# Performance work log

Hardware: AMD Instinct MI355X
Metric: run time of the kernel (lower is better)

## Reference

```python
import jax, jax.numpy as jnp
import numpy as np

N_NODES = 100000
N_EDGES = 3200000
D_FEAT = 256
TOP_K = 50000


def setup_inputs() -> dict:
    key = jax.random.key(0)
    k1, k2, k3 = jax.random.split(key, 3)
    h = jax.random.normal(k1, (N_NODES, D_FEAT), dtype=jnp.float32)
    W = jax.random.normal(k2, (D_FEAT, 1), dtype=jnp.float32) * (1.0 / np.sqrt(D_FEAT))
    b = jnp.zeros((1,), dtype=jnp.float32)
    edge_index = jax.random.randint(k3, (2, N_EDGES), 0, N_NODES, dtype=jnp.int64)
    return {"h": h, "W": W, "b": b, "edge_index": edge_index, "top_k": TOP_K}


def reference(h, W, b, edge_index, top_k):
    # scores = sigmoid(Linear(h)) -> [N, 1]
    scores = jax.nn.sigmoid(h @ W + b)  # [N, 1]
    # top-k node selection by score (descending), like dgl.topk_nodes
    top_scores, node_ids = jax.lax.top_k(scores[:, 0], top_k)  # [k], [k]
    # gather features of selected nodes, scale by their scores
    new_h = h[node_ids] * top_scores[:, None]  # [k, d]
    # induced-subgraph edges: edge kept iff both endpoints selected
    member = jnp.zeros((h.shape[0],), dtype=bool).at[node_ids].set(True)
    edge_mask = member[edge_index[0]] & member[edge_index[1]]  # [E]
    return new_h, node_ids, edge_mask
```

## Files before the change

### kernel.cpp

```cpp
#include <hip/hip_runtime.h>
#include <math.h>

#define N_NODES 100000
#define D_FEAT  256
#define TOP_K   50000
#define NBINS   65536
#define NCHUNK  64
#define CUTPOS  (N_NODES - TOP_K)
#define ROWSTRIDE 260


__device__ __forceinline__ int bucket_of(float s) {
    int b = (int)(s * 65536.0f);
    return min(max(b, 0), NBINS - 1);
}

__device__ __forceinline__ float np_expf(float x) {
    float q  = rintf(x * 1.44269504088896341f);
    float xr = fmaf(-q, 0.693359375f, x);
    xr       = fmaf(-q, -2.12194440e-4f, xr);
    float x2 = xr * xr;
    float p  = 1.9875691500E-4f;
    p = fmaf(p, xr, 1.3981999507E-3f);
    p = fmaf(p, xr, 8.3334519073E-3f);
    p = fmaf(p, xr, 4.1665795894E-2f);
    p = fmaf(p, xr, 1.6666665459E-1f);
    p = fmaf(p, xr, 5.0000001201E-1f);
    p = fmaf(p, x2, xr);
    p = p + 1.0f;
    return ldexpf(p, (int)q);
}

__global__ void score_kernel(const float* __restrict__ h,
                             const float* __restrict__ W,
                             const float* __restrict__ bvec,
                             float* __restrict__ s32,
                             int* __restrict__ hist) {
    __shared__ float rows[32 * ROWSTRIDE];
    __shared__ float wl[256];
    int tid  = threadIdx.x;
    int wave = tid >> 6;
    int lane = tid & 63;
    int g    = lane >> 3;
    int l    = lane & 7;

    wl[tid] = W[tid];

    int nodeBase = blockIdx.x * 32 + wave * 8;
#pragma unroll
    for (int r = 0; r < 8; ++r) {
        float4 v = ((const float4*)(h + (size_t)(nodeBase + r) * D_FEAT))[lane];
        *((float4*)&rows[(wave * 8 + r) * ROWSTRIDE + lane * 4]) = v;
    }
    __syncthreads();

    float wreg[32];
#pragma unroll
    for (int i = 0; i < 32; ++i) wreg[i] = wl[i * 8 + l];

    const float* myrow = &rows[(wave * 8 + g) * ROWSTRIDE];
    float acc = 0.0f;
#pragma unroll
    for (int i = 0; i < 32; ++i)
        acc = fmaf(myrow[i * 8 + l], wreg[i], acc);

    float b01 = acc + __shfl_xor(acc, 1, 64);
    float b23 = b01 + __shfl_xor(b01, 2, 64);
    float z   = b23 + __shfl_xor(b23, 4, 64);

    z = z + bvec[0];
    float x = -z;
    float t = np_expf(x);
    float u = 1.0f + t;
    float s = 1.0f / u;

    if (l == 0) {
        int node = nodeBase + g;
        s32[node] = s;
        atomicAdd(&hist[bucket_of(s)], 1);
    }
}

__global__ void scan_chunks_kernel(const int* __restrict__ hist,
                                   int* __restrict__ offs,
                                   int* __restrict__ cursor,
                                   int* __restrict__ chunkSum) {
    __shared__ int wsum[4];
    int tid  = threadIdx.x;
    int lane = tid & 63;
    int wid  = tid >> 6;
    int base = blockIdx.x * 1024 + tid * 4;

    int4 hv = *((const int4*)(hist + base));
    int e1 = hv.x;
    int e2 = hv.x + hv.y;
    int e3 = e2 + hv.z;
    int tot = e3 + hv.w;

    int incl = tot;
#pragma unroll
    for (int d = 1; d < 64; d <<= 1) {
        int t = __shfl_up(incl, d, 64);
        if (lane >= d) incl += t;
    }
    if (lane == 63) wsum[wid] = incl;
    __syncthreads();
    int wbase = 0;
#pragma unroll
    for (int w = 0; w < 3; ++w)
        if (w < wid) wbase += wsum[w];

    int excl = wbase + (incl - tot);
    int4 ov = make_int4(excl, excl + e1, excl + e2, excl + e3);
    *((int4*)(offs + base))   = ov;
    *((int4*)(cursor + base)) = ov;
    if (tid == 255) chunkSum[blockIdx.x] = excl + tot;
}

__device__ __forceinline__ void build_base(const int* __restrict__ chunkSum,
                                           int* sbase, int tid) {
    if (tid < 64) {
        int v = chunkSum[tid];
        int inc = v;
#pragma unroll
        for (int d = 1; d < 64; d <<= 1) {
            int t = __shfl_up(inc, d, 64);
            if (tid >= d) inc += t;
        }
        sbase[tid] = inc - v;
    }
}

__global__ void scatter_kernel(const float* __restrict__ s32,
                               int* __restrict__ cursor,
                               const int* __restrict__ chunkSum,
                               float* __restrict__ ss,
                               int* __restrict__ si) {
    __shared__ int sbase[64];
    int tid = threadIdx.x;
    build_base(chunkSum, sbase, tid);
    __syncthreads();
    int i = blockIdx.x * 256 + tid;
    if (i >= N_NODES) return;
    float s = s32[i];
    int b = bucket_of(s);
    int pos = sbase[b >> 10] + atomicAdd(&cursor[b], 1);
    ss[pos] = s;
    si[pos] = i;
}

__global__ void bucket_sort_kernel(const int* __restrict__ offs,
                                   const int* __restrict__ chunkSum,
                                   float* __restrict__ ss,
                                   int* __restrict__ si) {
    __shared__ int sbase[65];
    int tid = threadIdx.x;
    build_base(chunkSum, sbase, tid);
    if (tid == 64) sbase[64] = N_NODES;
    __syncthreads();
    int b = blockIdx.x * 256 + tid;
    int s0 = sbase[b >> 10] + offs[b];
    int e  = (b == NBINS - 1) ? N_NODES : sbase[(b + 1) >> 10] + offs[b + 1];
    if (e <= CUTPOS || e - s0 < 2) return;
    for (int i = s0 + 1; i < e; ++i) {
        float ks = ss[i];
        int   ki = si[i];
        int j = i - 1;
        while (j >= s0) {
            float ps = ss[j];
            int   pi = si[j];
            bool gt = (ps > ks) || (ps == ks && pi < ki);
            if (!gt) break;
            ss[j + 1] = ps;
            si[j + 1] = pi;
            --j;
        }
        ss[j + 1] = ks;
        si[j + 1] = ki;
    }
}

__global__ void emit_gather_kernel(const float* __restrict__ h,
                                   const float* __restrict__ ss,
                                   const int* __restrict__ si,
                                   float* __restrict__ out_newh,
                                   float* __restrict__ out_ids,
                                   unsigned char* __restrict__ member) {
    int tid  = threadIdx.x;
    int row  = blockIdx.x * 4 + (tid >> 6);
    int lane = tid & 63;
    int p = N_NODES - 1 - row;
    int id  = si[p];
    float s = ss[p];
    if (lane == 0) {
        member[id]   = 1;
        out_ids[row] = (float)id;
    }
    const float4* hv = (const float4*)(h + (size_t)id * D_FEAT);
    float4 v = hv[lane];
    ((float4*)(out_newh + (size_t)row * D_FEAT))[lane] =
        make_float4(v.x * s, v.y * s, v.z * s, v.w * s);
}

__global__ void edge_kernel(const int* __restrict__ ei,
                            const unsigned char* __restrict__ member,
                            float* __restrict__ out_mask,
                            int E) {
    __shared__ int sflag;
    int tid = threadIdx.x;
    if (tid < 64) {
        int v = ei[2 * tid + 1];
        unsigned long long m = __ballot(v == 0);
        if (tid == 0) sflag = (m == ~0ULL) ? 1 : 0;
    }
    __syncthreads();
    int flag = sflag;

    int k  = blockIdx.x * 256 + tid;
    int i0 = 2 * k;
    int i1 = i0 + 1;
    if (i0 >= E) return;

    int s0, d0, s1 = 0, d1 = 0;
    if (i1 < E) {
        if (flag) {
            int4 a  = ((const int4*)ei)[k];
            int4 bq = ((const int4*)(ei + 2 * (size_t)E))[k];
            s0 = a.x;  s1 = a.z;
            d0 = bq.x; d1 = bq.z;
        } else {
            int2 a  = ((const int2*)ei)[k];
            int2 bq = ((const int2*)(ei + (size_t)E))[k];
            s0 = a.x;  s1 = a.y;
            d0 = bq.x; d1 = bq.y;
        }
    } else {
        if (flag) { s0 = ei[2 * i0]; d0 = ei[2 * ((size_t)E + i0)]; }
        else      { s0 = ei[i0];     d0 = ei[(size_t)E + i0]; }
    }

    bool ok0 = ((unsigned)s0 < (unsigned)N_NODES) &&
               ((unsigned)d0 < (unsigned)N_NODES) &&
               member[s0] && member[d0];
    out_mask[i0] = ok0 ? 1.0f : 0.0f;
    if (i1 < E) {
        bool ok1 = ((unsigned)s1 < (unsigned)N_NODES) &&
                   ((unsigned)d1 < (unsigned)N_NODES) &&
                   member[s1] && member[d1];
        out_mask[i1] = ok1 ? 1.0f : 0.0f;
    }
}

extern "C" void kernel_launch(void* const* d_in, const int* in_sizes, int n_in,
                              void* d_out, int out_size, void* d_ws, size_t ws_size,
                              hipStream_t stream) {
    const float* h  = (const float*)d_in[0];
    const float* W  = (const float*)d_in[1];
    const float* bv = (const float*)d_in[2];
    const int*   ei = (const int*)d_in[3];
    const int E = in_sizes[3] / 2;

    char* ws = (char*)d_ws;
    float*         s32      = (float*)(ws + 0);
    float*         ss       = (float*)(ws + 400000);
    int*           si       = (int*)(ws + 800000);
    int*           hist     = (int*)(ws + 1200000);
    unsigned char* member   = (unsigned char*)(ws + 1462144);
    int*           offs     = (int*)(ws + 1562144);
    int*           cursor   = (int*)(ws + 1824288);
    int*           chunkSum = (int*)(ws + 2086432);

    float* out      = (float*)d_out;
    float* out_newh = out;
    float* out_ids  = out + (size_t)TOP_K * D_FEAT;
    float* out_mask = out + (size_t)TOP_K * D_FEAT + TOP_K;

    hipMemsetAsync(ws + 1200000, 0, 362144, stream);

    score_kernel<<<N_NODES / 32, 256, 0, stream>>>(h, W, bv, s32, hist);
    scan_chunks_kernel<<<NCHUNK, 256, 0, stream>>>(hist, offs, cursor, chunkSum);
    scatter_kernel<<<(N_NODES + 255) / 256, 256, 0, stream>>>(s32, cursor, chunkSum, ss, si);
    bucket_sort_kernel<<<NBINS / 256, 256, 0, stream>>>(offs, chunkSum, ss, si);
    emit_gather_kernel<<<TOP_K / 4, 256, 0, stream>>>(h, ss, si, out_newh, out_ids, member);
    edge_kernel<<<(E / 2 + 255) / 256, 256, 0, stream>>>(ei, member, out_mask, E);
}
```

Baseline: 242.8 us.

## Fuse pipeline into cooperative persistent kernel with bitset membership and concurrent emit/edge

```diff
diff --git a/kernel.cpp b/kernel.cpp
--- a/kernel.cpp
+++ b/kernel.cpp
@@ -1,5 +1,8 @@
 #include <hip/hip_runtime.h>
+#include <hip/hip_cooperative_groups.h>
 #include <math.h>
+
+namespace cg = cooperative_groups;
 
 #define N_NODES 100000
 #define D_FEAT  256
@@ -8,6 +11,9 @@
 #define NCHUNK  64
 #define CUTPOS  (N_NODES - TOP_K)
 #define ROWSTRIDE 260
+#define GRID    1024
+#define EMIT_BLOCKS 640
+#define NBITW   3200
 
 
 __device__ __forceinline__ int bucket_of(float s) {
@@ -31,22 +37,21 @@
     return ldexpf(p, (int)q);
 }
 
-__global__ void score_kernel(const float* __restrict__ h,
-                             const float* __restrict__ W,
-                             const float* __restrict__ bvec,
-                             float* __restrict__ s32,
-                             int* __restrict__ hist) {
-    __shared__ float rows[32 * ROWSTRIDE];
-    __shared__ float wl[256];
-    int tid  = threadIdx.x;
+
+__device__ __forceinline__ void score_group(const float* __restrict__ h,
+                                            float bval,
+                                            float* __restrict__ s32,
+                                            int* __restrict__ hist,
+                                            float* rows,
+                                            const float* wreg,
+                                            int tid, int grp) {
     int wave = tid >> 6;
     int lane = tid & 63;
     int g    = lane >> 3;
     int l    = lane & 7;
-
-    wl[tid] = W[tid];
-
-    int nodeBase = blockIdx.x * 32 + wave * 8;
+    int nodeBase = grp * 32 + wave * 8;
+
+    __syncthreads();
 #pragma unroll
     for (int r = 0; r < 8; ++r) {
         float4 v = ((const float4*)(h + (size_t)(nodeBase + r) * D_FEAT))[lane];
@@ -54,10 +59,6 @@
     }
     __syncthreads();
 
-    float wreg[32];
-#pragma unroll
-    for (int i = 0; i < 32; ++i) wreg[i] = wl[i * 8 + l];
-
     const float* myrow = &rows[(wave * 8 + g) * ROWSTRIDE];
     float acc = 0.0f;
 #pragma unroll
@@ -68,11 +69,9 @@
     float b23 = b01 + __shfl_xor(b01, 2, 64);
     float z   = b23 + __shfl_xor(b23, 4, 64);
 
-    z = z + bvec[0];
-    float x = -z;
-    float t = np_expf(x);
-    float u = 1.0f + t;
-    float s = 1.0f / u;
+    z = z + bval;
+    float t = np_expf(-z);
+    float s = 1.0f / (1.0f + t);
 
     if (l == 0) {
         int node = nodeBase + g;
@@ -81,15 +80,14 @@
     }
 }
 
-__global__ void scan_chunks_kernel(const int* __restrict__ hist,
-                                   int* __restrict__ offs,
-                                   int* __restrict__ cursor,
-                                   int* __restrict__ chunkSum) {
-    __shared__ int wsum[4];
-    int tid  = threadIdx.x;
+__device__ __forceinline__ void scan_chunk(const int* __restrict__ hist,
+                                           int* __restrict__ offs,
+                                           int* __restrict__ cursor,
+                                           int* __restrict__ chunkSum,
+                                           int* wsum, int cid, int tid) {
     int lane = tid & 63;
     int wid  = tid >> 6;
-    int base = blockIdx.x * 1024 + tid * 4;
+    int base = cid * 1024 + tid * 4;
 
     int4 hv = *((const int4*)(hist + base));
     int e1 = hv.x;
@@ -114,7 +112,7 @@
     int4 ov = make_int4(excl, excl + e1, excl + e2, excl + e3);
     *((int4*)(offs + base))   = ov;
     *((int4*)(cursor + base)) = ov;
-    if (tid == 255) chunkSum[blockIdx.x] = excl + tot;
+    if (tid == 255) chunkSum[cid] = excl + tot;
 }
 
 __device__ __forceinline__ void build_base(const int* __restrict__ chunkSum,
@@ -131,37 +129,32 @@
     }
 }
 
-__global__ void scatter_kernel(const float* __restrict__ s32,
-                               int* __restrict__ cursor,
-                               const int* __restrict__ chunkSum,
-                               float* __restrict__ ss,
-                               int* __restrict__ si) {
-    __shared__ int sbase[64];
-    int tid = threadIdx.x;
-    build_base(chunkSum, sbase, tid);
-    __syncthreads();
-    int i = blockIdx.x * 256 + tid;
-    if (i >= N_NODES) return;
+__device__ __forceinline__ void scatter_node(const float* __restrict__ s32,
+                                             int* __restrict__ cursor,
+                                             const int* __restrict__ offs,
+                                             const int* sbase,
+                                             unsigned int* __restrict__ bits,
+                                             float* __restrict__ ss,
+                                             int* __restrict__ si, int i) {
     float s = s32[i];
     int b = bucket_of(s);
-    int pos = sbase[b >> 10] + atomicAdd(&cursor[b], 1);
-    ss[pos] = s;
-    si[pos] = i;
-}
-
-__global__ void bucket_sort_kernel(const int* __restrict__ offs,
-                                   const int* __restrict__ chunkSum,
-                                   float* __restrict__ ss,
-                                   int* __restrict__ si) {
-    __shared__ int sbase[65];
-    int tid = threadIdx.x;
-    build_base(chunkSum, sbase, tid);
-    if (tid == 64) sbase[64] = N_NODES;
-    __syncthreads();
-    int b = blockIdx.x * 256 + tid;
+    int pos = atomicAdd(&cursor[b], 1);
+    int gbase = sbase[b >> 10];
+    int gpos = gbase + pos;
+    ss[gpos] = s;
+    si[gpos] = i;
+    if (gbase + offs[b] >= CUTPOS)
+        atomicOr(&bits[(unsigned)i >> 5], 1u << (i & 31));
+}
+
+__device__ __forceinline__ void sort_bucket(const int* __restrict__ offs,
+                                            const int* sbase,
+                                            unsigned int* __restrict__ bits,
+                                            float* __restrict__ ss,
+                                            int* __restrict__ si, int b) {
     int s0 = sbase[b >> 10] + offs[b];
     int e  = (b == NBINS - 1) ? N_NODES : sbase[(b + 1) >> 10] + offs[b + 1];
-    if (e <= CUTPOS || e - s0 < 2) return;
+    if (e <= CUTPOS) return;
     for (int i = s0 + 1; i < e; ++i) {
         float ks = ss[i];
         int   ki = si[i];
@@ -178,51 +171,43 @@
         ss[j + 1] = ks;
         si[j + 1] = ki;
     }
-}
-
-__global__ void emit_gather_kernel(const float* __restrict__ h,
-                                   const float* __restrict__ ss,
-                                   const int* __restrict__ si,
-                                   float* __restrict__ out_newh,
-                                   float* __restrict__ out_ids,
-                                   unsigned char* __restrict__ member) {
-    int tid  = threadIdx.x;
-    int row  = blockIdx.x * 4 + (tid >> 6);
-    int lane = tid & 63;
+    if (s0 < CUTPOS) {
+        for (int i = CUTPOS; i < e; ++i) {
+            int id = si[i];
+            atomicOr(&bits[(unsigned)id >> 5], 1u << (id & 31));
+        }
+    }
+}
+
+__device__ __forceinline__ void emit_row(const float* __restrict__ h,
+                                         const float* __restrict__ ss,
+                                         const int* __restrict__ si,
+                                         float* __restrict__ out_newh,
+                                         float* __restrict__ out_ids,
+                                         int row, int lane) {
     int p = N_NODES - 1 - row;
     int id  = si[p];
     float s = ss[p];
-    if (lane == 0) {
-        member[id]   = 1;
-        out_ids[row] = (float)id;
-    }
+    if (lane == 0) out_ids[row] = (float)id;
     const float4* hv = (const float4*)(h + (size_t)id * D_FEAT);
     float4 v = hv[lane];
     ((float4*)(out_newh + (size_t)row * D_FEAT))[lane] =
         make_float4(v.x * s, v.y * s, v.z * s, v.w * s);
 }
 
-__global__ void edge_kernel(const int* __restrict__ ei,
-                            const unsigned char* __restrict__ member,
-                            float* __restrict__ out_mask,
-                            int E) {
-    __shared__ int sflag;
-    int tid = threadIdx.x;
-    if (tid < 64) {
-        int v = ei[2 * tid + 1];
-        unsigned long long m = __ballot(v == 0);
-        if (tid == 0) sflag = (m == ~0ULL) ? 1 : 0;
-    }
-    __syncthreads();
-    int flag = sflag;
-
-    int k  = blockIdx.x * 256 + tid;
+__device__ __forceinline__ unsigned mem_bit(const unsigned int* __restrict__ bits,
+                                            int s) {
+    return (bits[(unsigned)s >> 5] >> (s & 31)) & 1u;
+}
+
+__device__ __forceinline__ void edge_pair(const int* __restrict__ ei,
+                                          const unsigned int* __restrict__ bits,
+                                          float* __restrict__ out_mask,
+                                          int E, int flag, int k) {
     int i0 = 2 * k;
     int i1 = i0 + 1;
-    if (i0 >= E) return;
-
-    int s0, d0, s1 = 0, d1 = 0;
     if (i1 < E) {
+        int s0, d0, s1, d1;
         if (flag) {
             int4 a  = ((const int4*)ei)[k];
             int4 bq = ((const int4*)(ei + 2 * (size_t)E))[k];
@@ -234,21 +219,164 @@
             s0 = a.x;  s1 = a.y;
             d0 = bq.x; d1 = bq.y;
         }
+        bool ok0 = ((unsigned)s0 < (unsigned)N_NODES) &&
+                   ((unsigned)d0 < (unsigned)N_NODES) &&
+                   mem_bit(bits, s0) && mem_bit(bits, d0);
+        bool ok1 = ((unsigned)s1 < (unsigned)N_NODES) &&
+                   ((unsigned)d1 < (unsigned)N_NODES) &&
+                   mem_bit(bits, s1) && mem_bit(bits, d1);
+        ((float2*)out_mask)[k] = make_float2(ok0 ? 1.0f : 0.0f, ok1 ? 1.0f : 0.0f);
     } else {
+        int s0, d0;
         if (flag) { s0 = ei[2 * i0]; d0 = ei[2 * ((size_t)E + i0)]; }
         else      { s0 = ei[i0];     d0 = ei[(size_t)E + i0]; }
-    }
-
-    bool ok0 = ((unsigned)s0 < (unsigned)N_NODES) &&
-               ((unsigned)d0 < (unsigned)N_NODES) &&
-               member[s0] && member[d0];
-    out_mask[i0] = ok0 ? 1.0f : 0.0f;
-    if (i1 < E) {
-        bool ok1 = ((unsigned)s1 < (unsigned)N_NODES) &&
-                   ((unsigned)d1 < (unsigned)N_NODES) &&
-                   member[s1] && member[d1];
-        out_mask[i1] = ok1 ? 1.0f : 0.0f;
-    }
+        bool ok0 = ((unsigned)s0 < (unsigned)N_NODES) &&
+                   ((unsigned)d0 < (unsigned)N_NODES) &&
+                   mem_bit(bits, s0) && mem_bit(bits, d0);
+        out_mask[i0] = ok0 ? 1.0f : 0.0f;
+    }
+}
+
+__global__ __launch_bounds__(256, 4) void mega_kernel(
+        const float* __restrict__ h, const float* __restrict__ W,
+        const float* __restrict__ bvec, const int* __restrict__ ei, int E,
+        float* __restrict__ s32, float* __restrict__ ss, int* __restrict__ si,
+        int* __restrict__ hist, unsigned int* __restrict__ bits,
+        int* __restrict__ offs, int* __restrict__ cursor,
+        int* __restrict__ chunkSum,
+        float* __restrict__ out_newh, float* __restrict__ out_ids,
+        float* __restrict__ out_mask) {
+    __shared__ float rows[32 * ROWSTRIDE];
+    __shared__ float wl[256];
+    __shared__ int   wsum[4];
+    __shared__ int   sbase[64];
+    __shared__ int   sflag;
+
+    cg::grid_group grid = cg::this_grid();
+    int tid  = threadIdx.x;
+    int bid  = blockIdx.x;
+    int gtid = bid * 256 + tid;
+
+    if (gtid < NBINS) hist[gtid] = 0;
+    if (gtid < NBITW) bits[gtid] = 0;
+
+    wl[tid] = W[tid];
+    __syncthreads();
+    int l = tid & 7;
+    float wreg[32];
+#pragma unroll
+    for (int i = 0; i < 32; ++i) wreg[i] = wl[i * 8 + l];
+    float bval = bvec[0];
+
+    grid.sync();
+
+    for (int grp = bid; grp < N_NODES / 32; grp += GRID)
+        score_group(h, bval, s32, hist, rows, wreg, tid, grp);
+
+    grid.sync();
+
+    if (bid < NCHUNK) scan_chunk(hist, offs, cursor, chunkSum, wsum, bid, tid);
+
+    grid.sync();
+
+    build_base(chunkSum, sbase, tid);
+    __syncthreads();
+    if (gtid < N_NODES) scatter_node(s32, cursor, offs, sbase, bits, ss, si, gtid);
+
+    grid.sync();
+
+    if (gtid < NBINS) sort_bucket(offs, sbase, bits, ss, si, gtid);
+
+    grid.sync();
+
+    int lane = tid & 63;
+    if (bid < EMIT_BLOCKS) {
+        int wgid = bid * 4 + (tid >> 6);
+        for (int row = wgid; row < TOP_K; row += EMIT_BLOCKS * 4)
+            emit_row(h, ss, si, out_newh, out_ids, row, lane);
+    } else {
+        if (tid < 64) {
+            int v = ei[2 * tid + 1];
+            unsigned long long m = __ballot(v == 0);
+            if (tid == 0) sflag = (m == ~0ULL) ? 1 : 0;
+        }
+        __syncthreads();
+        int flag = sflag;
+        int npairs = (E + 1) / 2;
+        int t0 = (bid - EMIT_BLOCKS) * 256 + tid;
+        for (int k = t0; k < npairs; k += (GRID - EMIT_BLOCKS) * 256)
+            edge_pair(ei, bits, out_mask, E, flag, k);
+    }
+}
+
+
+__global__ void f_score(const float* __restrict__ h, const float* __restrict__ W,
+                        const float* __restrict__ bvec,
+                        float* __restrict__ s32, int* __restrict__ hist) {
+    __shared__ float rows[32 * ROWSTRIDE];
+    __shared__ float wl[256];
+    int tid = threadIdx.x;
+    wl[tid] = W[tid];
+    __syncthreads();
+    int l = tid & 7;
+    float wreg[32];
+#pragma unroll
+    for (int i = 0; i < 32; ++i) wreg[i] = wl[i * 8 + l];
+    score_group(h, bvec[0], s32, hist, rows, wreg, tid, blockIdx.x);
+}
+
+__global__ void f_scan(const int* __restrict__ hist, int* __restrict__ offs,
+                       int* __restrict__ cursor, int* __restrict__ chunkSum) {
+    __shared__ int wsum[4];
+    scan_chunk(hist, offs, cursor, chunkSum, wsum, blockIdx.x, threadIdx.x);
+}
+
+__global__ void f_scatter(const float* __restrict__ s32, int* __restrict__ cursor,
+                          const int* __restrict__ offs,
+                          const int* __restrict__ chunkSum,
+                          unsigned int* __restrict__ bits,
+                          float* __restrict__ ss, int* __restrict__ si) {
+    __shared__ int sbase[64];
+    int tid = threadIdx.x;
+    build_base(chunkSum, sbase, tid);
+    __syncthreads();
+    int i = blockIdx.x * 256 + tid;
+    if (i < N_NODES) scatter_node(s32, cursor, offs, sbase, bits, ss, si, i);
+}
+
+__global__ void f_sort(const int* __restrict__ offs,
+                       const int* __restrict__ chunkSum,
+                       unsigned int* __restrict__ bits,
+                       float* __restrict__ ss, int* __restrict__ si) {
+    __shared__ int sbase[64];
+    int tid = threadIdx.x;
+    build_base(chunkSum, sbase, tid);
+    __syncthreads();
+    int b = blockIdx.x * 256 + tid;
+    if (b < NBINS) sort_bucket(offs, sbase, bits, ss, si, b);
+}
+
+__global__ void f_emit(const float* __restrict__ h, const float* __restrict__ ss,
+                       const int* __restrict__ si, float* __restrict__ out_newh,
+                       float* __restrict__ out_ids) {
+    int tid = threadIdx.x;
+    int row = blockIdx.x * 4 + (tid >> 6);
+    if (row < TOP_K) emit_row(h, ss, si, out_newh, out_ids, row, tid & 63);
+}
+
+__global__ void f_edge(const int* __restrict__ ei,
+                       const unsigned int* __restrict__ bits,
+                       float* __restrict__ out_mask, int E) {
+    __shared__ int sflag;
+    int tid = threadIdx.x;
+    if (tid < 64) {
+        int v = ei[2 * tid + 1];
+        unsigned long long m = __ballot(v == 0);
+        if (tid == 0) sflag = (m == ~0ULL) ? 1 : 0;
+    }
+    __syncthreads();
+    int k = blockIdx.x * 256 + tid;
+    if (k < (E + 1) / 2) edge_pair(ei, bits, out_mask, E, sflag, k);
 }
 
 extern "C" void kernel_launch(void* const* d_in, const int* in_sizes, int n_in,
@@ -258,29 +386,38 @@
     const float* W  = (const float*)d_in[1];
     const float* bv = (const float*)d_in[2];
     const int*   ei = (const int*)d_in[3];
-    const int E = in_sizes[3] / 2;
+    int E = in_sizes[3] / 2;
 
     char* ws = (char*)d_ws;
-    float*         s32      = (float*)(ws + 0);
-    float*         ss       = (float*)(ws + 400000);
-    int*           si       = (int*)(ws + 800000);
-    int*           hist     = (int*)(ws + 1200000);
-    unsigned char* member   = (unsigned char*)(ws + 1462144);
-    int*           offs     = (int*)(ws + 1562144);
-    int*           cursor   = (int*)(ws + 1824288);
-    int*           chunkSum = (int*)(ws + 2086432);
+    float*        s32      = (float*)(ws + 0);
+    float*        ss       = (float*)(ws + 400000);
+    int*          si       = (int*)(ws + 800000);
+    int*          hist     = (int*)(ws + 1200000);
+    unsigned int* bits     = (unsigned int*)(ws + 1462144);
+    int*          offs     = (int*)(ws + 1562144);
+    int*          cursor   = (int*)(ws + 1824288);
+    int*          chunkSum = (int*)(ws + 2086432);
 
     float* out      = (float*)d_out;
     float* out_newh = out;
     float* out_ids  = out + (size_t)TOP_K * D_FEAT;
     float* out_mask = out + (size_t)TOP_K * D_FEAT + TOP_K;
 
-    hipMemsetAsync(ws + 1200000, 0, 362144, stream);
-
-    score_kernel<<<N_NODES / 32, 256, 0, stream>>>(h, W, bv, s32, hist);
-    scan_chunks_kernel<<<NCHUNK, 256, 0, stream>>>(hist, offs, cursor, chunkSum);
-    scatter_kernel<<<(N_NODES + 255) / 256, 256, 0, stream>>>(s32, cursor, chunkSum, ss, si);
-    bucket_sort_kernel<<<NBINS / 256, 256, 0, stream>>>(offs, chunkSum, ss, si);
-    emit_gather_kernel<<<TOP_K / 4, 256, 0, stream>>>(h, ss, si, out_newh, out_ids, member);
-    edge_kernel<<<(E / 2 + 255) / 256, 256, 0, stream>>>(ei, member, out_mask, E);
-}
+    void* args[] = { (void*)&h, (void*)&W, (void*)&bv, (void*)&ei, (void*)&E,
+                     (void*)&s32, (void*)&ss, (void*)&si, (void*)&hist,
+                     (void*)&bits, (void*)&offs, (void*)&cursor, (void*)&chunkSum,
+                     (void*)&out_newh, (void*)&out_ids, (void*)&out_mask };
+
+    hipError_t err = hipLaunchCooperativeKernel(mega_kernel, dim3(GRID), dim3(256),
+                                                args, 0, stream);
+    if (err != hipSuccess) {
+        hipMemsetAsync(ws + 1200000, 0, 274944, stream);
+        f_score<<<N_NODES / 32, 256, 0, stream>>>(h, W, bv, s32, hist);
+        f_scan<<<NCHUNK, 256, 0, stream>>>(hist, offs, cursor, chunkSum);
+        f_scatter<<<(N_NODES + 255) / 256, 256, 0, stream>>>(s32, cursor, offs,
+                                                             chunkSum, bits, ss, si);
+        f_sort<<<NBINS / 256, 256, 0, stream>>>(offs, chunkSum, bits, ss, si);
+        f_emit<<<TOP_K / 4, 256, 0, stream>>>(h, ss, si, out_newh, out_ids);
+        f_edge<<<((E + 1) / 2 + 255) / 256, 256, 0, stream>>>(ei, bits, out_mask, E);
+    }
+}
```

New measurement: 747.5 us. +207.9%, slower.

## Build membership bitmask during scatter and fuse gather with edge mask

Applied to the files above, without the earlier changes.

```diff
diff --git a/kernel.cpp b/kernel.cpp
--- a/kernel.cpp
+++ b/kernel.cpp
@@ -8,6 +8,9 @@
 #define NCHUNK  64
 #define CUTPOS  (N_NODES - TOP_K)
 #define ROWSTRIDE 260
+#define NBITW   3200
+#define FUSE_GRID   2048
+#define EMIT_BLOCKS 1280
 
 
 __device__ __forceinline__ int bucket_of(float s) {
@@ -69,10 +72,8 @@
     float z   = b23 + __shfl_xor(b23, 4, 64);
 
     z = z + bvec[0];
-    float x = -z;
-    float t = np_expf(x);
-    float u = 1.0f + t;
-    float s = 1.0f / u;
+    float t = np_expf(-z);
+    float s = 1.0f / (1.0f + t);
 
     if (l == 0) {
         int node = nodeBase + g;
@@ -133,7 +134,9 @@
 
 __global__ void scatter_kernel(const float* __restrict__ s32,
                                int* __restrict__ cursor,
+                               const int* __restrict__ offs,
                                const int* __restrict__ chunkSum,
+                               unsigned int* __restrict__ bits,
                                float* __restrict__ ss,
                                int* __restrict__ si) {
     __shared__ int sbase[64];
@@ -144,24 +147,27 @@
     if (i >= N_NODES) return;
     float s = s32[i];
     int b = bucket_of(s);
-    int pos = sbase[b >> 10] + atomicAdd(&cursor[b], 1);
-    ss[pos] = s;
-    si[pos] = i;
+    int pos = atomicAdd(&cursor[b], 1);
+    int gbase = sbase[b >> 10];
+    ss[gbase + pos] = s;
+    si[gbase + pos] = i;
+    if (gbase + offs[b] >= CUTPOS)
+        atomicOr(&bits[(unsigned)i >> 5], 1u << (i & 31));
 }
 
 __global__ void bucket_sort_kernel(const int* __restrict__ offs,
                                    const int* __restrict__ chunkSum,
+                                   unsigned int* __restrict__ bits,
                                    float* __restrict__ ss,
                                    int* __restrict__ si) {
-    __shared__ int sbase[65];
+    __shared__ int sbase[64];
     int tid = threadIdx.x;
     build_base(chunkSum, sbase, tid);
-    if (tid == 64) sbase[64] = N_NODES;
     __syncthreads();
     int b = blockIdx.x * 256 + tid;
     int s0 = sbase[b >> 10] + offs[b];
     int e  = (b == NBINS - 1) ? N_NODES : sbase[(b + 1) >> 10] + offs[b + 1];
-    if (e <= CUTPOS || e - s0 < 2) return;
+    if (e <= CUTPOS) return;
     for (int i = s0 + 1; i < e; ++i) {
         float ks = ss[i];
         int   ki = si[i];
@@ -178,36 +184,48 @@
         ss[j + 1] = ks;
         si[j + 1] = ki;
     }
-}
-
-__global__ void emit_gather_kernel(const float* __restrict__ h,
-                                   const float* __restrict__ ss,
-                                   const int* __restrict__ si,
-                                   float* __restrict__ out_newh,
-                                   float* __restrict__ out_ids,
-                                   unsigned char* __restrict__ member) {
-    int tid  = threadIdx.x;
-    int row  = blockIdx.x * 4 + (tid >> 6);
-    int lane = tid & 63;
-    int p = N_NODES - 1 - row;
-    int id  = si[p];
-    float s = ss[p];
-    if (lane == 0) {
-        member[id]   = 1;
-        out_ids[row] = (float)id;
-    }
-    const float4* hv = (const float4*)(h + (size_t)id * D_FEAT);
-    float4 v = hv[lane];
-    ((float4*)(out_newh + (size_t)row * D_FEAT))[lane] =
-        make_float4(v.x * s, v.y * s, v.z * s, v.w * s);
-}
-
-__global__ void edge_kernel(const int* __restrict__ ei,
-                            const unsigned char* __restrict__ member,
-                            float* __restrict__ out_mask,
-                            int E) {
+    if (s0 < CUTPOS) {
+        for (int i = CUTPOS; i < e; ++i) {
+            int id = si[i];
+            atomicOr(&bits[(unsigned)id >> 5], 1u << (id & 31));
+        }
+    }
+}
+
+__device__ __forceinline__ unsigned mem_bit(const unsigned int* __restrict__ bits,
+                                            int s) {
+    return (bits[(unsigned)s >> 5] >> (s & 31)) & 1u;
+}
+
+__global__ void emit_edge_kernel(const float* __restrict__ h,
+                                 const float* __restrict__ ss,
+                                 const int* __restrict__ si,
+                                 const int* __restrict__ ei,
+                                 const unsigned int* __restrict__ bits,
+                                 float* __restrict__ out_newh,
+                                 float* __restrict__ out_ids,
+                                 float* __restrict__ out_mask,
+                                 int E) {
+    int tid = threadIdx.x;
+    int bid = blockIdx.x;
+
+    if (bid < EMIT_BLOCKS) {
+        int lane = tid & 63;
+        int wg   = bid * 4 + (tid >> 6);
+        for (int row = wg; row < TOP_K; row += EMIT_BLOCKS * 4) {
+            int p = N_NODES - 1 - row;
+            int id  = si[p];
+            float s = ss[p];
+            if (lane == 0) out_ids[row] = (float)id;
+            const float4* hv = (const float4*)(h + (size_t)id * D_FEAT);
+            float4 v = hv[lane];
+            ((float4*)(out_newh + (size_t)row * D_FEAT))[lane] =
+                make_float4(v.x * s, v.y * s, v.z * s, v.w * s);
+        }
+        return;
+    }
+
     __shared__ int sflag;
-    int tid = threadIdx.x;
     if (tid < 64) {
         int v = ei[2 * tid + 1];
         unsigned long long m = __ballot(v == 0);
@@ -216,38 +234,41 @@
     __syncthreads();
     int flag = sflag;
 
-    int k  = blockIdx.x * 256 + tid;
-    int i0 = 2 * k;
-    int i1 = i0 + 1;
-    if (i0 >= E) return;
-
-    int s0, d0, s1 = 0, d1 = 0;
-    if (i1 < E) {
-        if (flag) {
-            int4 a  = ((const int4*)ei)[k];
-            int4 bq = ((const int4*)(ei + 2 * (size_t)E))[k];
-            s0 = a.x;  s1 = a.z;
-            d0 = bq.x; d1 = bq.z;
+    int npairs = (E + 1) / 2;
+    int stride = (FUSE_GRID - EMIT_BLOCKS) * 256;
+    for (int k = (bid - EMIT_BLOCKS) * 256 + tid; k < npairs; k += stride) {
+        int i0 = 2 * k;
+        int i1 = i0 + 1;
+        if (i1 < E) {
+            int s0, d0, s1, d1;
+            if (flag) {
+                int4 a  = ((const int4*)ei)[k];
+                int4 bq = ((const int4*)(ei + 2 * (size_t)E))[k];
+                s0 = a.x;  s1 = a.z;
+                d0 = bq.x; d1 = bq.z;
+            } else {
+                int2 a  = ((const int2*)ei)[k];
+                int2 bq = ((const int2*)(ei + (size_t)E))[k];
+                s0 = a.x;  s1 = a.y;
+                d0 = bq.x; d1 = bq.y;
+            }
+            bool ok0 = ((unsigned)s0 < (unsigned)N_NODES) &&
+                       ((unsigned)d0 < (unsigned)N_NODES) &&
+                       mem_bit(bits, s0) && mem_bit(bits, d0);
+            bool ok1 = ((unsigned)s1 < (unsigned)N_NODES) &&
+                       ((unsigned)d1 < (unsigned)N_NODES) &&
+                       mem_bit(bits, s1) && mem_bit(bits, d1);
+            ((float2*)out_mask)[k] = make_float2(ok0 ? 1.0f : 0.0f,
+                                                 ok1 ? 1.0f : 0.0f);
         } else {
-            int2 a  = ((const int2*)ei)[k];
-            int2 bq = ((const int2*)(ei + (size_t)E))[k];
-            s0 = a.x;  s1 = a.y;
-            d0 = bq.x; d1 = bq.y;
-        }
-    } else {
-        if (flag) { s0 = ei[2 * i0]; d0 = ei[2 * ((size_t)E + i0)]; }
-        else      { s0 = ei[i0];     d0 = ei[(size_t)E + i0]; }
-    }
-
-    bool ok0 = ((unsigned)s0 < (unsigned)N_NODES) &&
-               ((unsigned)d0 < (unsigned)N_NODES) &&
-               member[s0] && member[d0];
-    out_mask[i0] = ok0 ? 1.0f : 0.0f;
-    if (i1 < E) {
-        bool ok1 = ((unsigned)s1 < (unsigned)N_NODES) &&
-                   ((unsigned)d1 < (unsigned)N_NODES) &&
-                   member[s1] && member[d1];
-        out_mask[i1] = ok1 ? 1.0f : 0.0f;
+            int s0, d0;
+            if (flag) { s0 = ei[2 * i0]; d0 = ei[2 * ((size_t)E + i0)]; }
+            else      { s0 = ei[i0];     d0 = ei[(size_t)E + i0]; }
+            bool ok0 = ((unsigned)s0 < (unsigned)N_NODES) &&
+                       ((unsigned)d0 < (unsigned)N_NODES) &&
+                       mem_bit(bits, s0) && mem_bit(bits, d0);
+            out_mask[i0] = ok0 ? 1.0f : 0.0f;
+        }
     }
 }
 
@@ -261,26 +282,27 @@
     const int E = in_sizes[3] / 2;
 
     char* ws = (char*)d_ws;
-    float*         s32      = (float*)(ws + 0);
-    float*         ss       = (float*)(ws + 400000);
-    int*           si       = (int*)(ws + 800000);
-    int*           hist     = (int*)(ws + 1200000);
-    unsigned char* member   = (unsigned char*)(ws + 1462144);
-    int*           offs     = (int*)(ws + 1562144);
-    int*           cursor   = (int*)(ws + 1824288);
-    int*           chunkSum = (int*)(ws + 2086432);
+    float*        s32      = (float*)(ws + 0);
+    float*        ss       = (float*)(ws + 400000);
+    int*          si       = (int*)(ws + 800000);
+    int*          hist     = (int*)(ws + 1200000);
+    unsigned int* bits     = (unsigned int*)(ws + 1462144);
+    int*          offs     = (int*)(ws + 1562144);
+    int*          cursor   = (int*)(ws + 1824288);
+    int*          chunkSum = (int*)(ws + 2086432);
 
     float* out      = (float*)d_out;
     float* out_newh = out;
     float* out_ids  = out + (size_t)TOP_K * D_FEAT;
     float* out_mask = out + (size_t)TOP_K * D_FEAT + TOP_K;
 
-    hipMemsetAsync(ws + 1200000, 0, 362144, stream);
+    hipMemsetAsync(ws + 1200000, 0, 274944, stream);
 
     score_kernel<<<N_NODES / 32, 256, 0, stream>>>(h, W, bv, s32, hist);
     scan_chunks_kernel<<<NCHUNK, 256, 0, stream>>>(hist, offs, cursor, chunkSum);
-    scatter_kernel<<<(N_NODES + 255) / 256, 256, 0, stream>>>(s32, cursor, chunkSum, ss, si);
-    bucket_sort_kernel<<<NBINS / 256, 256, 0, stream>>>(offs, chunkSum, ss, si);
-    emit_gather_kernel<<<TOP_K / 4, 256, 0, stream>>>(h, ss, si, out_newh, out_ids, member);
-    edge_kernel<<<(E / 2 + 255) / 256, 256, 0, stream>>>(ei, member, out_mask, E);
-}
+    scatter_kernel<<<(N_NODES + 255) / 256, 256, 0, stream>>>(s32, cursor, offs,
+                                                              chunkSum, bits, ss, si);
+    bucket_sort_kernel<<<NBINS / 256, 256, 0, stream>>>(offs, chunkSum, bits, ss, si);
+    emit_edge_kernel<<<FUSE_GRID, 256, 0, stream>>>(h, ss, si, ei, bits,
+                                                    out_newh, out_ids, out_mask, E);
+}
```

Result: no change. 245.8 us (+1.2%).
